# Kernel tuning notes

Measured on AMD Instinct MI355X. Metric: run time of the kernel, lower is better.

The kernel has to match this reference:

```python
import jax, jax.numpy as jnp
import numpy as np

P = 16  # patch_size


def setup_inputs() -> dict:
    key = jax.random.key(0)
    k1, k2 = jax.random.split(key)
    B, N, C = 128, P * P, 768
    x = jax.random.normal(k1, (B, N, C), dtype=jnp.float32)
    # learned spectral filter: (P, P//2+1, C, 2) real/imag pairs, init ~ N(0, 0.02^2)
    complex_weight = jax.random.normal(k2, (P, P // 2 + 1, C, 2), dtype=jnp.float32) * 0.02
    return {"x": x, "complex_weight": complex_weight}


def reference(x, complex_weight):
    dtype = x.dtype
    xf = x.astype(jnp.float32)
    B, N, C = xf.shape
    xf = xf.reshape(B, P, P, C)
    # 2D real FFT over spatial dims with orthonormal scaling -> [B, P, P//2+1, C] complex
    Xf = jnp.fft.rfft2(xf, axes=(1, 2), norm="ortho")
    weight = jax.lax.complex(complex_weight[..., 0], complex_weight[..., 1])  # [P, P//2+1, C]
    Xf = Xf * weight  # broadcast over batch
    out = jnp.fft.irfft2(Xf, s=(P, P), axes=(1, 2), norm="ortho")
    return out.reshape(B, N, C).astype(dtype)
```

## Files before the change

kernel.cpp:

```cpp
#include <hip/hip_runtime.h>


constexpr int PP = 16;
constexpr int NS = 256;
constexpr int CH = 768;
constexpr int NB = 128;

__global__ void gf_build_k(const float* __restrict__ w, float* __restrict__ kbuf) {
    __shared__ float ct[16], st[16];
    if (threadIdx.x < 16) {
        const float ang = 6.28318530717958647692f * (float)threadIdx.x * (1.0f / 16.0f);
        ct[threadIdx.x] = cosf(ang);
        st[threadIdx.x] = sinf(ang);
    }
    __syncthreads();

    const int pq = blockIdx.x;
    const int c  = blockIdx.y * blockDim.x + threadIdx.x;
    const int p = pq >> 4, q = pq & 15;

    float acc = 0.0f;
#pragma unroll 1
    for (int u = 0; u < 16; ++u) {
        const float* wu = w + (size_t)(u * 9) * 2 * CH + 2 * c;
#pragma unroll
        for (int v = 0; v < 9; ++v) {
            const float cv = (v == 0 || v == 8) ? 1.0f : 2.0f;
            const int t = (u * p + v * q) & 15;
            const float wr = wu[(size_t)v * 2 * CH];
            const float wi = wu[(size_t)v * 2 * CH + 1];
            acc += cv * (wr * ct[t] - wi * st[t]);
        }
    }
    kbuf[pq * CH + c] = acc * (1.0f / 256.0f);
}

__global__ __launch_bounds__(128, 2) void gf_conv(const float* __restrict__ x,
                                                  const float* __restrict__ kbuf,
                                                  float* __restrict__ out) {
    __shared__ __align__(16) float xs[NS][32];
    __shared__ __align__(16) float ks[NS][32];

    const int b   = blockIdx.y;
    const int c0  = blockIdx.x * 32;
    const int tid = threadIdx.x;

    {
        const int ch4 = (tid & 7) << 2;
        const int sr  = tid >> 3;
        const float* xb = x + (size_t)b * NS * CH + c0;
        const float* kb = kbuf + c0;
#pragma unroll
        for (int i = 0; i < 16; ++i) {
            const int s = (i << 4) + sr;
            *(float4*)&xs[s][ch4] = *(const float4*)(xb + (size_t)s * CH + ch4);
            *(float4*)&ks[s][ch4] = *(const float4*)(kb + (size_t)s * CH + ch4);
        }
    }
    __syncthreads();

    const int ch = (tid & 7) << 2;
    const int n  = tid >> 3;

    float4 acc[16];
#pragma unroll
    for (int m = 0; m < 16; ++m) acc[m] = make_float4(0.f, 0.f, 0.f, 0.f);

#pragma unroll 1
    for (int qq = 0; qq < 16; ++qq) {
        const int q = (qq + n) & 15;
        const int j = (n - q) & 15;

        float4 kv[16];
#pragma unroll
        for (int p = 0; p < 16; ++p)
            kv[p] = *(const float4*)&ks[(p << 4) | q][ch];

#pragma unroll
        for (int d = 0; d < 16; ++d) {
            const float4 xx = *(const float4*)&xs[(d << 4) + j][ch];
#pragma unroll
            for (int p = 0; p < 16; ++p) {
                const int m = (p + d) & 15;
                acc[m].x = fmaf(kv[p].x, xx.x, acc[m].x);
                acc[m].y = fmaf(kv[p].y, xx.y, acc[m].y);
                acc[m].z = fmaf(kv[p].z, xx.z, acc[m].z);
                acc[m].w = fmaf(kv[p].w, xx.w, acc[m].w);
            }
        }
    }

    float* ob = out + (size_t)b * NS * CH + c0 + ch;
#pragma unroll
    for (int m = 0; m < 16; ++m)
        *(float4*)(ob + (size_t)((m << 4) + n) * CH) = acc[m];
}

extern "C" void kernel_launch(void* const* d_in, const int* in_sizes, int n_in,
                              void* d_out, int out_size, void* d_ws, size_t ws_size,
                              hipStream_t stream) {
    const float* x = (const float*)d_in[0];
    const float* w = (const float*)d_in[1];
    float* out  = (float*)d_out;
    float* kbuf = (float*)d_ws;

    gf_build_k<<<dim3(256, 3), 256, 0, stream>>>(w, kbuf);
    gf_conv<<<dim3(CH / 32, NB), 128, 0, stream>>>(x, kbuf, out);
}
```

Before: 299.5 us.

## Stream x columns via async global-to-LDS double buffering, share kernel tile across batches

Each block now handles two batch items with 256 threads and shares one LDS copy of the spatial kernel tile between them. Instead of staging the whole x tile up front, it streams only the single x column needed per iteration into a double-buffered LDS slot. The loads use global_load_lds, which writes straight from global memory into LDS without going through registers. The goals are lower LDS use per batch, higher occupancy, and load latency hidden behind the FMA loop, at the cost of a block barrier every iteration.

```diff
diff --git a/kernel.cpp b/kernel.cpp
--- a/kernel.cpp
+++ b/kernel.cpp
@@ -5,6 +5,12 @@
 constexpr int NS = 256;
 constexpr int CH = 768;
 constexpr int NB = 128;
+
+__device__ __forceinline__ void cp_g2s_16(const void* g, void* s) {
+    __builtin_amdgcn_global_load_lds(
+        (const __attribute__((address_space(1))) void*)g,
+        (__attribute__((address_space(3))) void*)s, 16, 0, 0);
+}
 
 __global__ void gf_build_k(const float* __restrict__ w, float* __restrict__ kbuf) {
     __shared__ float ct[16], st[16];
@@ -35,32 +41,40 @@
     kbuf[pq * CH + c] = acc * (1.0f / 256.0f);
 }
 
-__global__ __launch_bounds__(128, 2) void gf_conv(const float* __restrict__ x,
+__global__ __launch_bounds__(256, 3) void gf_conv(const float* __restrict__ x,
                                                   const float* __restrict__ kbuf,
                                                   float* __restrict__ out) {
-    __shared__ __align__(16) float xs[NS][32];
     __shared__ __align__(16) float ks[NS][32];
+    __shared__ __align__(16) float xcol[2][2][16][32];
 
-    const int b   = blockIdx.y;
-    const int c0  = blockIdx.x * 32;
-    const int tid = threadIdx.x;
+    const int tid  = threadIdx.x;
+    const int half = tid >> 7;
+    const int b    = (blockIdx.y << 1) | half;
+    const int c0   = blockIdx.x * 32;
+    const int wave = tid >> 6;
+    const int idx  = tid & 127;
+    const int dr   = idx >> 3;
+    const int ch4  = (idx & 7) << 2;
+
+    const float* xb = x + (size_t)b * NS * CH + c0;
 
     {
-        const int ch4 = (tid & 7) << 2;
-        const int sr  = tid >> 3;
-        const float* xb = x + (size_t)b * NS * CH + c0;
+        const int srow = tid >> 3;
+        const int kch4 = (tid & 7) << 2;
         const float* kb = kbuf + c0;
+        float* lbase = &ks[0][0] + wave * 256;
 #pragma unroll
-        for (int i = 0; i < 16; ++i) {
-            const int s = (i << 4) + sr;
-            *(float4*)&xs[s][ch4] = *(const float4*)(xb + (size_t)s * CH + ch4);
-            *(float4*)&ks[s][ch4] = *(const float4*)(kb + (size_t)s * CH + ch4);
-        }
+        for (int i = 0; i < 8; ++i)
+            cp_g2s_16(kb + (size_t)(i * 32 + srow) * CH + kch4, lbase + i * 1024);
+    }
+    {
+        float* lbase = &xcol[0][half][0][0] + (wave & 1) * 256;
+        cp_g2s_16(xb + (size_t)(dr * 16 + 0) * CH + ch4, lbase);
     }
     __syncthreads();
 
-    const int ch = (tid & 7) << 2;
-    const int n  = tid >> 3;
+    const int chq = (tid & 7) << 2;
+    const int n   = (tid >> 3) & 15;
 
     float4 acc[16];
 #pragma unroll
@@ -68,17 +82,22 @@
 
 #pragma unroll 1
     for (int qq = 0; qq < 16; ++qq) {
+        {
+            float* lbase = &xcol[(qq + 1) & 1][half][0][0] + (wave & 1) * 256;
+            cp_g2s_16(xb + (size_t)(dr * 16 + ((15 - qq) & 15)) * CH + ch4, lbase);
+        }
+
         const int q = (qq + n) & 15;
-        const int j = (n - q) & 15;
+        const float4* xrow = (const float4*)&xcol[qq & 1][half][0][chq];
 
         float4 kv[16];
 #pragma unroll
         for (int p = 0; p < 16; ++p)
-            kv[p] = *(const float4*)&ks[(p << 4) | q][ch];
+            kv[p] = *(const float4*)&ks[(p << 4) | q][chq];
 
 #pragma unroll
         for (int d = 0; d < 16; ++d) {
-            const float4 xx = *(const float4*)&xs[(d << 4) + j][ch];
+            const float4 xx = xrow[d * 8];
 #pragma unroll
             for (int p = 0; p < 16; ++p) {
                 const int m = (p + d) & 15;
@@ -88,9 +107,10 @@
                 acc[m].w = fmaf(kv[p].w, xx.w, acc[m].w);
             }
         }
+        __syncthreads();
     }
 
-    float* ob = out + (size_t)b * NS * CH + c0 + ch;
+    float* ob = out + (size_t)b * NS * CH + c0 + chq;
 #pragma unroll
     for (int m = 0; m < 16; ++m)
         *(float4*)(ob + (size_t)((m << 4) + n) * CH) = acc[m];
@@ -105,5 +125,5 @@
     float* kbuf = (float*)d_ws;
 
     gf_build_k<<<dim3(256, 3), 256, 0, stream>>>(w, kbuf);
-    gf_conv<<<dim3(CH / 32, NB), 128, 0, stream>>>(x, kbuf, out);
+    gf_conv<<<dim3(CH / 32, NB / 2), 256, 0, stream>>>(x, kbuf, out);
 }
```

Result: faster. 281.1 us (-6.2%).
